# Kernel optimization log

Measured on AMD Instinct MI355X. Metric: run time of the kernel, lower is better.

The kernel has to match this reference:

```python
import jax, jax.numpy as jnp
import numpy as np

B, N, D, H, V, L = 32, 64, 128, 256, 32000, 3  # batch, nodes, embd_dim, msg_hid, vocab, num_layers


def _linear_init(key, fan_in, fan_out):
    k1, k2 = jax.random.split(key)
    s = 1.0 / np.sqrt(fan_in)
    W = jax.random.uniform(k1, (fan_out, fan_in), jnp.float32, -s, s)
    b = jax.random.uniform(k2, (fan_out,), jnp.float32, -s, s)
    return W, b


def setup_inputs() -> dict:
    key = jax.random.key(0)
    ks = jax.random.split(key, 7)
    x = jax.random.randint(ks[0], (B, N), 0, V)                      # token ids
    arcs = jax.random.randint(ks[1], (B, N, N), 0, 2).astype(jnp.int32)
    lengths = jnp.ones((B, N), dtype=jnp.int32)                      # unused by forward
    embd_table = jax.random.normal(ks[2], (V, D), jnp.float32)
    embd_table = embd_table.at[0].set(0.0)                           # padding_idx = 0
    W1_0, b1_0 = _linear_init(ks[3], 2 * D, H)
    W2_0, b2_0 = _linear_init(ks[4], H, D)
    W1_1, b1_1 = _linear_init(ks[5], 2 * D, H)
    W2_1, b2_1 = _linear_init(ks[6], H, D)
    return dict(x=x, arcs=arcs, lengths=lengths, embd_table=embd_table,
                W1_0=W1_0, b1_0=b1_0, W2_0=W2_0, b2_0=b2_0,
                W1_1=W1_1, b1_1=b1_1, W2_1=W2_1, b2_1=b2_1)


def reference(x, arcs, lengths, embd_table,
              W1_0, b1_0, W2_0, b2_0, W1_1, b1_1, W2_1, b2_1):
    # Edge k = (row=k//n, col=k%n). Caller passes senders_idxs=one_hot(cols),
    # receivers_idxs=one_hot(rows); aggregation sums messages over rows.
    # Equivalent gather/scatter expressed as (B,n,n,·) broadcast + sum over axis 2.
    b, n = x.shape
    d = embd_table.shape[1]
    E = embd_table[x]                                   # (B,n,d)
    a = arcs.astype(E.dtype)[..., None]                 # (B,n,n,1) edge-type-1 weight

    def mlp(pre, W1, b1, W2, b2):
        h = jax.nn.relu(jnp.einsum('brce,he->brch', pre, W1) + b1)
        return jax.nn.relu(jnp.einsum('brch,dh->brcd', h, W2) + b2)

    for _ in range(L):
        senders = jnp.broadcast_to(E[:, None, :, :], (b, n, n, d))    # col embedding
        receivers = jnp.broadcast_to(E[:, :, None, :], (b, n, n, d))  # row embedding
        pre = jnp.concatenate([senders, receivers], axis=-1)          # (B,n,n,2d)
        m0 = mlp(pre, W1_0, b1_0, W2_0, b2_0)
        m1 = mlp(pre, W1_1, b1_1, W2_1, b2_1)
        all_msgs = m0 * (1.0 - a) + m1 * a                            # (B,n,n,d)
        agg = all_msgs.sum(axis=2)                                    # scatter-add over rows
        E = E + agg
    return E[:, 0, :]
```

## Files before the change

kernel.cpp:

```cpp
#include <hip/hip_runtime.h>
#include <hip/hip_bf16.h>
#include <stdint.h>


#define NB 32
#define NN 64
#define DD 128
#define HH 256

typedef __attribute__((ext_vector_type(4))) float f32x4;
typedef __attribute__((ext_vector_type(8))) _Float16 f16x8;

__device__ __forceinline__ uint64_t cvt4h(f32x4 v) {
  union { _Float16 h[4]; uint64_t u; } x;
  x.h[0] = (_Float16)v[0]; x.h[1] = (_Float16)v[1];
  x.h[2] = (_Float16)v[2]; x.h[3] = (_Float16)v[3];
  return x.u;
}

__global__ __launch_bounds__(256) void k_setup(const int* __restrict__ x,
                                               const float* __restrict__ table,
                                               float* __restrict__ E0,
                                               const float* __restrict__ W1_0,
                                               const float* __restrict__ W1_1,
                                               const float* __restrict__ W2_0,
                                               const float* __restrict__ W2_1,
                                               _Float16* __restrict__ W1fp,
                                               _Float16* __restrict__ W2fp) {
  int bid = blockIdx.x, t = threadIdx.x;
  if (bid < 256) {
    int i = bid * 256 + t;
    int node = i >> 5;
    ((f32x4*)E0)[i] = ((const f32x4*)table)[(size_t)x[node] * 32 + (i & 31)];
  } else {
    int tid = (bid - 256) * 256 + t;
    const float* src; uint64_t* dst; int off;
    if (tid < 32768) {
      src = (tid < 16384) ? W1_0 : W1_1;
      off = tid & 16383;
      dst = (uint64_t*)W1fp + (tid >> 14) * 16384 + off;
    } else {
      int t2 = tid - 32768;
      src = (t2 < 8192) ? W2_0 : W2_1;
      off = t2 & 8191;
      dst = (uint64_t*)W2fp + (t2 >> 13) * 8192 + off;
    }
    *dst = cvt4h(((const f32x4*)src)[off]);
  }
}

template <int NSP, int NR>
__global__ __launch_bounds__(256) void k_fused(
    const float* __restrict__ E0,
    const float* __restrict__ spA,
    const float* __restrict__ spB,
    float* __restrict__ spOut,
    const _Float16* __restrict__ W1fp,
    const _Float16* __restrict__ W2fp,
    const float* __restrict__ b1_0, const float* __restrict__ b1_1,
    const float* __restrict__ b2_0, const float* __restrict__ b2_1,
    const int* __restrict__ arcs) {
  __shared__ char lds[32768];
  char* Els_c = lds;
  char* Els_r = lds + 8192;
  char* Tsl   = lds + 12288;
  char* Trl   = lds + 28672;

  int t = threadIdx.x;
  int rg = blockIdx.x, b = blockIdx.y;
  int p = blockIdx.z >> 1, ch = blockIdx.z & 1;
  int rbase = rg * NR;
  int lane = t & 63, w = t >> 6, col = lane & 15, khi = lane >> 4;
  const f32x4 z4 = {0.f, 0.f, 0.f, 0.f};

  {
    const float* eb = E0 + (size_t)b * NN * DD;
#pragma unroll
    for (int ii = 0; ii < 6; ++ii) {
      int chunk = ii * 256 + t;
      int lrow = chunk >> 5, ck = chunk & 31;
      int node; char* dst;
      if (lrow < 32) {
        node = ch * 32 + lrow;
        dst = Els_c + lrow * 256;
      } else {
        int lr = lrow - 32;
        int nr = rbase + lr; if (nr > 63) nr = 63;
        node = nr;
        dst = Els_r + lr * 256;
      }
      f32x4 v = ((const f32x4*)(eb + node * DD))[ck];
      if (NSP >= 1) {
#pragma unroll
        for (int s = 0; s < 4; ++s)
          v += ((const f32x4*)(spA + ((size_t)(s * NB + b) * NN + node) * DD))[ck];
      }
      if (NSP >= 2) {
#pragma unroll
        for (int s = 0; s < 4; ++s)
          v += ((const f32x4*)(spB + ((size_t)(s * NB + b) * NN + node) * DD))[ck];
      }
      *(uint64_t*)(dst + ((ck * 8) ^ ((lrow & 7) << 4))) = cvt4h(v);
    }
  }
  __syncthreads();

  const _Float16* Wq = W1fp + p * 65536;
  const float* b1p = p ? b1_1 : b1_0;

#pragma unroll
  for (int nth = 0; nth < 2; ++nth) {
    f16x8 bfr[2][4];
#pragma unroll
    for (int nt = 0; nt < 2; ++nt) {
      int h = w * 64 + nth * 32 + nt * 16 + col;
#pragma unroll
      for (int ks = 0; ks < 4; ++ks)
        bfr[nt][ks] = *(const f16x8*)(Wq + h * 256 + ks * 32 + khi * 8);
    }
    f32x4 tacc[2][2];
#pragma unroll
    for (int mt = 0; mt < 2; ++mt) { tacc[mt][0] = z4; tacc[mt][1] = z4; }
#pragma unroll
    for (int ks = 0; ks < 4; ++ks) {
      f16x8 a[2];
#pragma unroll
      for (int mt = 0; mt < 2; ++mt) {
        int c = mt * 16 + col;
        a[mt] = *(const f16x8*)(Els_c + c * 256 +
                                ((ks * 64 + khi * 16) ^ ((c & 7) << 4)));
      }
#pragma unroll
      for (int mt = 0; mt < 2; ++mt) {
        tacc[mt][0] = __builtin_amdgcn_mfma_f32_16x16x32_f16(a[mt], bfr[0][ks],
                                                             tacc[mt][0], 0, 0, 0);
        tacc[mt][1] = __builtin_amdgcn_mfma_f32_16x16x32_f16(a[mt], bfr[1][ks],
                                                             tacc[mt][1], 0, 0, 0);
      }
    }
#pragma unroll
    for (int mt = 0; mt < 2; ++mt)
#pragma unroll
      for (int nt = 0; nt < 2; ++nt) {
        int h = w * 64 + nth * 32 + nt * 16 + col;
#pragma unroll
        for (int j = 0; j < 4; ++j) {
          int c = mt * 16 + khi * 4 + j;
          *(_Float16*)(Tsl + c * 512 + ((h * 2) ^ ((c & 7) << 4))) =
              (_Float16)tacc[mt][nt][j];
        }
      }
  }
#pragma unroll
  for (int nth = 0; nth < 2; ++nth) {
    f16x8 bfrR[2][4];
#pragma unroll
    for (int nt = 0; nt < 2; ++nt) {
      int h = w * 64 + nth * 32 + nt * 16 + col;
#pragma unroll
      for (int ks = 0; ks < 4; ++ks)
        bfrR[nt][ks] = *(const f16x8*)(Wq + h * 256 + 128 + ks * 32 + khi * 8);
    }
    f32x4 taccR[2] = {z4, z4};
#pragma unroll
    for (int ks = 0; ks < 4; ++ks) {
      f16x8 ar = *(const f16x8*)(Els_r + col * 256 +
                                 ((ks * 64 + khi * 16) ^ ((col & 7) << 4)));
      taccR[0] = __builtin_amdgcn_mfma_f32_16x16x32_f16(ar, bfrR[0][ks],
                                                        taccR[0], 0, 0, 0);
      taccR[1] = __builtin_amdgcn_mfma_f32_16x16x32_f16(ar, bfrR[1][ks],
                                                        taccR[1], 0, 0, 0);
    }
    if (khi < 2) {
#pragma unroll
      for (int nt = 0; nt < 2; ++nt) {
        int h = w * 64 + nth * 32 + nt * 16 + col;
        float bb = b1p[h];
#pragma unroll
        for (int j = 0; j < 4; ++j) {
          int lr = khi * 4 + j;
          *(_Float16*)(Trl + lr * 512 + ((h * 2) ^ ((lr & 7) << 4))) =
              (_Float16)(taccR[nt][j] + bb);
        }
      }
    }
  }
  __syncthreads();

  int d0 = w * 32 + col;
  const _Float16* W2p = W2fp + p * 32768;
  f16x8 bv[2][8];
#pragma unroll
  for (int nt = 0; nt < 2; ++nt)
#pragma unroll
    for (int ks = 0; ks < 8; ++ks)
      bv[nt][ks] = *(const f16x8*)(W2p + (d0 + nt * 16) * 256 + ks * 32 + khi * 8);
  const float* b2p = p ? b2_1 : b2_0;
  float b2v[2] = {b2p[d0], b2p[d0 + 16]};

#pragma unroll 1
  for (int r = 0; r < NR; ++r) {
    f32x4 acc[2][2];
#pragma unroll
    for (int mt = 0; mt < 2; ++mt) { acc[mt][0] = z4; acc[mt][1] = z4; }
#pragma unroll
    for (int ks = 0; ks < 8; ++ks) {
      f16x8 trv = *(const f16x8*)(Trl + r * 512 +
                                  ((ks * 64 + khi * 16) ^ ((r & 7) << 4)));
#pragma unroll
      for (int mt = 0; mt < 2; ++mt) {
        int c = mt * 16 + col;
        f16x8 ts = *(const f16x8*)(Tsl + c * 512 +
                                   ((ks * 64 + khi * 16) ^ ((c & 7) << 4)));
        f16x8 zv = {};
        f16x8 a = __builtin_elementwise_max(ts + trv, zv);
        acc[mt][0] = __builtin_amdgcn_mfma_f32_16x16x32_f16(a, bv[0][ks],
                                                            acc[mt][0], 0, 0, 0);
        acc[mt][1] = __builtin_amdgcn_mfma_f32_16x16x32_f16(a, bv[1][ks],
                                                            acc[mt][1], 0, 0, 0);
      }
    }
    int rr = rbase + r;
    const int* arow = arcs + ((size_t)(b * NN + rr)) * NN + ch * 32;
    float s0 = 0.f, s1 = 0.f;
#pragma unroll
    for (int mt = 0; mt < 2; ++mt) {
      const int4 av = *(const int4*)(arow + mt * 16 + khi * 4);
#pragma unroll
      for (int j = 0; j < 4; ++j) {
        int ai = (j == 0) ? av.x : (j == 1) ? av.y : (j == 2) ? av.z : av.w;
        float wgt = p ? (float)ai : 1.0f - (float)ai;
        s0 = fmaf(wgt, fmaxf(acc[mt][0][j] + b2v[0], 0.f), s0);
        s1 = fmaf(wgt, fmaxf(acc[mt][1][j] + b2v[1], 0.f), s1);
      }
    }
    s0 += __shfl_xor(s0, 16); s0 += __shfl_xor(s0, 32);
    s1 += __shfl_xor(s1, 16); s1 += __shfl_xor(s1, 32);
    if (khi == 0) {
      int slice = p * 2 + ch;
      float* o = (NR == 1)
          ? spOut + (size_t)(slice * NB + b) * DD
          : spOut + ((size_t)(slice * NB + b) * NN + rr) * DD;
      o[d0] = s0; o[d0 + 16] = s1;
    }
  }
}

__global__ __launch_bounds__(256) void k_out(const float* __restrict__ E0,
                                             const float* __restrict__ spA,
                                             const float* __restrict__ spB,
                                             const float* __restrict__ spC,
                                             float* __restrict__ out) {
  int i = blockIdx.x * 256 + threadIdx.x;
  int b = i >> 7, d = i & 127;
  float acc = E0[(size_t)b * NN * DD + d];
#pragma unroll
  for (int s = 0; s < 4; ++s) {
    acc += spA[(size_t)(s * NB + b) * NN * DD + d];
    acc += spB[(size_t)(s * NB + b) * NN * DD + d];
    acc += spC[(size_t)(s * NB + b) * DD + d];
  }
  out[i] = acc;
}

extern "C" void kernel_launch(void* const* d_in, const int* in_sizes, int n_in,
                              void* d_out, int out_size, void* d_ws, size_t ws_size,
                              hipStream_t stream) {
  const int* x       = (const int*)d_in[0];
  const int* arcs    = (const int*)d_in[1];
  const float* table = (const float*)d_in[3];
  const float* W1_0  = (const float*)d_in[4];
  const float* b1_0  = (const float*)d_in[5];
  const float* W2_0  = (const float*)d_in[6];
  const float* b2_0  = (const float*)d_in[7];
  const float* W1_1  = (const float*)d_in[8];
  const float* b1_1  = (const float*)d_in[9];
  const float* W2_1  = (const float*)d_in[10];
  const float* b2_1  = (const float*)d_in[11];
  float* out = (float*)d_out;

  char* ws = (char*)d_ws;
  float* E0        = (float*)ws;
  _Float16* W1fp   = (_Float16*)(ws + (1u << 20));
  _Float16* W2fp   = (_Float16*)(ws + (1u << 20) + (256u << 10));
  float* SpA       = (float*)(ws + (2u << 20));
  float* SpB       = (float*)(ws + (6u << 20));
  float* SpC       = (float*)(ws + (10u << 20));

  k_setup<<<448, 256, 0, stream>>>(x, table, E0, W1_0, W1_1, W2_0, W2_1,
                                   W1fp, W2fp);
  k_fused<0, 8><<<dim3(8, 32, 4), 256, 0, stream>>>(
      E0, E0, E0, SpA, W1fp, W2fp, b1_0, b1_1, b2_0, b2_1, arcs);
  k_fused<1, 8><<<dim3(8, 32, 4), 256, 0, stream>>>(
      E0, SpA, E0, SpB, W1fp, W2fp, b1_0, b1_1, b2_0, b2_1, arcs);
  k_fused<2, 1><<<dim3(1, 32, 4), 256, 0, stream>>>(
      E0, SpA, SpB, SpC, W1fp, W2fp, b1_0, b1_1, b2_0, b2_1, arcs);
  k_out<<<16, 256, 0, stream>>>(E0, SpA, SpB, SpC, out);
}
```

Before: 111.4 us.

## Split embedding partial-sum reduction into separate fp16 pre-pass kernel

Moves the reduction of the base embedding plus per-chunk partial sums and the fp16 conversion out of each fused block into a small standalone kernel that writes an fp16 embedding buffer once per layer. The fused kernel now reads its A operands straight from global fp16 memory instead of staging them in swizzled LDS, and its shared memory shrinks from 32 KB to 20 KB. This removes the work each block repeated by reading and summing up to nine fp32 copies of the same rows. In exchange it adds three extra kernel launches and uncoalesced global operand loads inside the MFMA loops.

```diff
diff --git a/kernel.cpp b/kernel.cpp
--- a/kernel.cpp
+++ b/kernel.cpp
@@ -49,22 +49,36 @@
   }
 }
 
-template <int NSP, int NR>
+template <int NSP>
+__global__ __launch_bounds__(256) void k_esum(const float* __restrict__ E0,
+                                              const float* __restrict__ spA,
+                                              const float* __restrict__ spB,
+                                              _Float16* __restrict__ E16) {
+  int i = blockIdx.x * 256 + threadIdx.x;
+  f32x4 v = ((const f32x4*)E0)[i];
+  if (NSP >= 1) {
+#pragma unroll
+    for (int s = 0; s < 4; ++s) v += ((const f32x4*)spA)[s * 65536 + i];
+  }
+  if (NSP >= 2) {
+#pragma unroll
+    for (int s = 0; s < 4; ++s) v += ((const f32x4*)spB)[s * 65536 + i];
+  }
+  ((uint64_t*)E16)[i] = cvt4h(v);
+}
+
+template <int NR>
 __global__ __launch_bounds__(256) void k_fused(
-    const float* __restrict__ E0,
-    const float* __restrict__ spA,
-    const float* __restrict__ spB,
+    const _Float16* __restrict__ E16,
     float* __restrict__ spOut,
     const _Float16* __restrict__ W1fp,
     const _Float16* __restrict__ W2fp,
     const float* __restrict__ b1_0, const float* __restrict__ b1_1,
     const float* __restrict__ b2_0, const float* __restrict__ b2_1,
     const int* __restrict__ arcs) {
-  __shared__ char lds[32768];
-  char* Els_c = lds;
-  char* Els_r = lds + 8192;
-  char* Tsl   = lds + 12288;
-  char* Trl   = lds + 28672;
+  __shared__ char lds[20480];
+  char* Tsl = lds;
+  char* Trl = lds + 16384;
 
   int t = threadIdx.x;
   int rg = blockIdx.x, b = blockIdx.y;
@@ -72,38 +86,7 @@
   int rbase = rg * NR;
   int lane = t & 63, w = t >> 6, col = lane & 15, khi = lane >> 4;
   const f32x4 z4 = {0.f, 0.f, 0.f, 0.f};
-
-  {
-    const float* eb = E0 + (size_t)b * NN * DD;
-#pragma unroll
-    for (int ii = 0; ii < 6; ++ii) {
-      int chunk = ii * 256 + t;
-      int lrow = chunk >> 5, ck = chunk & 31;
-      int node; char* dst;
-      if (lrow < 32) {
-        node = ch * 32 + lrow;
-        dst = Els_c + lrow * 256;
-      } else {
-        int lr = lrow - 32;
-        int nr = rbase + lr; if (nr > 63) nr = 63;
-        node = nr;
-        dst = Els_r + lr * 256;
-      }
-      f32x4 v = ((const f32x4*)(eb + node * DD))[ck];
-      if (NSP >= 1) {
-#pragma unroll
-        for (int s = 0; s < 4; ++s)
-          v += ((const f32x4*)(spA + ((size_t)(s * NB + b) * NN + node) * DD))[ck];
-      }
-      if (NSP >= 2) {
-#pragma unroll
-        for (int s = 0; s < 4; ++s)
-          v += ((const f32x4*)(spB + ((size_t)(s * NB + b) * NN + node) * DD))[ck];
-      }
-      *(uint64_t*)(dst + ((ck * 8) ^ ((lrow & 7) << 4))) = cvt4h(v);
-    }
-  }
-  __syncthreads();
+  const _Float16* Eb = E16 + (size_t)b * NN * DD;
 
   const _Float16* Wq = W1fp + p * 65536;
   const float* b1p = p ? b1_1 : b1_0;
@@ -126,9 +109,8 @@
       f16x8 a[2];
 #pragma unroll
       for (int mt = 0; mt < 2; ++mt) {
-        int c = mt * 16 + col;
-        a[mt] = *(const f16x8*)(Els_c + c * 256 +
-                                ((ks * 64 + khi * 16) ^ ((c & 7) << 4)));
+        int node = ch * 32 + mt * 16 + col;
+        a[mt] = *(const f16x8*)(Eb + node * DD + ks * 32 + khi * 8);
       }
 #pragma unroll
       for (int mt = 0; mt < 2; ++mt) {
@@ -164,8 +146,8 @@
     f32x4 taccR[2] = {z4, z4};
 #pragma unroll
     for (int ks = 0; ks < 4; ++ks) {
-      f16x8 ar = *(const f16x8*)(Els_r + col * 256 +
-                                 ((ks * 64 + khi * 16) ^ ((col & 7) << 4)));
+      int node = rbase + col; if (node > 63) node = 63;
+      f16x8 ar = *(const f16x8*)(Eb + node * DD + ks * 32 + khi * 8);
       taccR[0] = __builtin_amdgcn_mfma_f32_16x16x32_f16(ar, bfrR[0][ks],
                                                         taccR[0], 0, 0, 0);
       taccR[1] = __builtin_amdgcn_mfma_f32_16x16x32_f16(ar, bfrR[1][ks],
@@ -283,17 +265,21 @@
   float* E0        = (float*)ws;
   _Float16* W1fp   = (_Float16*)(ws + (1u << 20));
   _Float16* W2fp   = (_Float16*)(ws + (1u << 20) + (256u << 10));
+  _Float16* E16    = (_Float16*)(ws + (1u << 20) + (384u << 10));
   float* SpA       = (float*)(ws + (2u << 20));
   float* SpB       = (float*)(ws + (6u << 20));
   float* SpC       = (float*)(ws + (10u << 20));
 
   k_setup<<<448, 256, 0, stream>>>(x, table, E0, W1_0, W1_1, W2_0, W2_1,
                                    W1fp, W2fp);
-  k_fused<0, 8><<<dim3(8, 32, 4), 256, 0, stream>>>(
-      E0, E0, E0, SpA, W1fp, W2fp, b1_0, b1_1, b2_0, b2_1, arcs);
-  k_fused<1, 8><<<dim3(8, 32, 4), 256, 0, stream>>>(
-      E0, SpA, E0, SpB, W1fp, W2fp, b1_0, b1_1, b2_0, b2_1, arcs);
-  k_fused<2, 1><<<dim3(1, 32, 4), 256, 0, stream>>>(
-      E0, SpA, SpB, SpC, W1fp, W2fp, b1_0, b1_1, b2_0, b2_1, arcs);
+  k_esum<0><<<256, 256, 0, stream>>>(E0, E0, E0, E16);
+  k_fused<8><<<dim3(8, 32, 4), 256, 0, stream>>>(
+      E16, SpA, W1fp, W2fp, b1_0, b1_1, b2_0, b2_1, arcs);
+  k_esum<1><<<256, 256, 0, stream>>>(E0, SpA, E0, E16);
+  k_fused<8><<<dim3(8, 32, 4), 256, 0, stream>>>(
+      E16, SpB, W1fp, W2fp, b1_0, b1_1, b2_0, b2_1, arcs);
+  k_esum<2><<<256, 256, 0, stream>>>(E0, SpA, SpB, E16);
+  k_fused<1><<<dim3(1, 32, 4), 256, 0, stream>>>(
+      E16, SpC, W1fp, W2fp, b1_0, b1_1, b2_0, b2_1, arcs);
   k_out<<<16, 256, 0, stream>>>(E0, SpA, SpB, SpC, out);
 }
```

New measurement: 118.5 us. 1.06x slower.
